# Optimization experiments

Hardware: AMD Instinct MI355X
Metric: run time of the kernel (lower is better)

## Reference

```python
import jax, jax.numpy as jnp
import numpy as np
from jax import lax

KSIZE = 3      # match kernel
STRIDE = 1
RATE = 2       # dilation / downscale rate
FUSE_K = 3     # diagonal-fuse kernel
SCALE = 10.0   # softmax scale
FUSE = True
ESC = 1e-4     # escape_NaN, added per-element before the reduce_sum (as in torch code)


def _same_pad(x, k, s):
    # x: [C, H, W] -> zero-padded so that strided k-window 'same' extraction works
    C, H, W = x.shape
    oh, ow = -(-H // s), -(-W // s)
    ph = max(0, (oh - 1) * s + k - H)
    pw = max(0, (ow - 1) * s + k - W)
    xp = jnp.pad(x, ((0, 0), (ph // 2, ph - ph // 2), (pw // 2, pw - pw // 2)))
    return xp, oh, ow


def extract_patches(x, k, s):
    # x: [C, H, W] -> [L, C, k, k], L row-major over output grid (matches torch Unfold)
    C = x.shape[0]
    xp, oh, ow = _same_pad(x, k, s)
    cols = [xp[:, dh:dh + s * (oh - 1) + 1:s, dw:dw + s * (ow - 1) + 1:s]
            for dh in range(k) for dw in range(k)]
    p = jnp.stack(cols, 0).reshape(k, k, C, oh, ow)
    return p.transpose(3, 4, 2, 0, 1).reshape(oh * ow, C, k, k)


def fuse_diag(x):
    # conv with eye(FUSE_K) kernel, 'same' padding: sum of diagonal shifts
    A, B = x.shape
    pt = (FUSE_K - 1) // 2
    pb = FUSE_K - 1 - pt
    xp = jnp.pad(x, ((pt, pb), (pt, pb)))
    out = xp[0:A, 0:B]
    for d in range(1, FUSE_K):
        out = out + xp[d:d + A, d:d + B]
    return out


def _forward(f, b, mask):
    B, C, H, W = f.shape
    kernel = 2 * RATE
    # mask -> mm gate over background patches (shared across batch: torch uses m[0])
    mask_s = mask[0][:, ::4 * RATE, ::4 * RATE]           # [1, H/r, W/r] nearest downsample
    m = extract_patches(mask_s, KSIZE, STRIDE)            # [L, 1, k, k]
    mm = (jnp.mean(m, axis=(1, 2, 3)) == 0.0).astype(f.dtype)[:, None, None]  # [L,1,1]

    def single(fi, bi):
        # raw patches from full-res background for reconstruction: [Lb, C, 2r, 2r]
        raw_w = extract_patches(bi, kernel, RATE * STRIDE)
        # nearest 1/rate downsample
        fs = fi[:, ::RATE, ::RATE]
        bs = bi[:, ::RATE, ::RATE]
        bh, bw = bs.shape[1], bs.shape[2]
        fh, fw = fs.shape[1], fs.shape[2]
        Lb, Lf = bh * bw, fh * fw
        # match patches from downsampled background, L2-normalized per patch
        w = extract_patches(bs, KSIZE, STRIDE)                      # [Lb, C, 3, 3]
        denom = jnp.sqrt(jnp.sum(w * w + ESC, axis=(1, 2, 3), keepdims=True))
        wn = (w / denom).reshape(Lb, -1)                            # [Lb, C*9]
        # correlation = conv of fs with wn filters = patch GEMM
        fp = extract_patches(fs, KSIZE, 1).reshape(Lf, -1)          # [Lf, C*9]
        scores = wn @ fp.T                                          # [Lb, Lf]
        if FUSE:
            s = fuse_diag(scores)
            s = s.reshape(bh, bw, fh, fw).transpose(1, 0, 3, 2).reshape(Lb, Lf)
            s = fuse_diag(s)
            s = s.reshape(bw, bh, fw, fh).transpose(1, 0, 3, 2).reshape(Lb, Lf)
            scores = s
        att = scores.reshape(Lb, fh, fw) * mm
        att = jax.nn.softmax(att * SCALE, axis=0) * mm              # softmax over patches
        # conv_transpose2d(att, raw_w, stride=rate, padding=1) / 4
        rhs = jnp.flip(raw_w, (2, 3)).transpose(1, 0, 2, 3)         # [C, Lb, 2r, 2r] OIHW
        pad = kernel - 1 - 1                                        # k - 1 - torch_padding
        out = lax.conv_general_dilated(
            att[None], rhs, window_strides=(1, 1),
            padding=[(pad, pad), (pad, pad)], lhs_dilation=(RATE, RATE),
            dimension_numbers=('NCHW', 'OIHW', 'NCHW'))[0] / 4.0    # [C, H, W]
        return out

    return jax.vmap(single)(f, b)


def setup_inputs() -> dict:
    key = jax.random.key(0)
    k1, k2 = jax.random.split(key)
    B, C, H, W = 4, 128, 96, 96
    f = jax.random.normal(k1, (B, C, H, W), jnp.float32)
    b = jax.random.normal(k2, (B, C, H, W), jnp.float32)
    mask = jnp.zeros((1, 1, 4 * H, 4 * W), jnp.float32)
    mask = mask.at[:, :, 96:288, 96:288].set(1.0)
    return {"f": f, "b": b, "mask": mask}


def reference(f, b, mask):
    return _forward(f, b, mask)
```

## Files before the change

kernel.cpp:

```cpp
#include <hip/hip_runtime.h>

typedef _Float16 half8 __attribute__((ext_vector_type(8)));
typedef float floatx4 __attribute__((ext_vector_type(4)));

#define LBF 2304
#define K1  1152
#define LDK2 2304

__device__ __forceinline__ void gll16(const _Float16* g, _Float16* l) {
    __builtin_amdgcn_global_load_lds((const __attribute__((address_space(1))) void*)g,
                                     (__attribute__((address_space(3))) void*)l, 16, 0, 0);
}

__device__ __forceinline__ int dec_kc(int s) { return (s >= 0) ? s + 1 : -s - 1; }

__global__ void prep_fp(const float* __restrict__ f, _Float16* __restrict__ fp) {
    int k = blockIdx.x * 128 + threadIdx.x;
    int p = blockIdx.y;
    int b = blockIdx.z;
    int c = k / 9, r = k % 9, u = r / 3, v = r % 3;
    int pi = p / 48, pj = p % 48;
    int y = pi - 1 + u, x = pj - 1 + v;
    float val = 0.f;
    if ((unsigned)y < 48u && (unsigned)x < 48u)
        val = f[(((long)b * 128 + c) * 96 + 2 * y) * 96 + 2 * x];
    fp[((long)b * LBF + p) * K1 + k] = (_Float16)val;
}

__global__ void prep_wn(const float* __restrict__ bsrc, _Float16* __restrict__ wn) {
    int p = blockIdx.x, b = blockIdx.y;
    int tid = threadIdx.x;
    int pi = p / 48, pj = p % 48;
    float w[9];
    float ss = 0.f;
#pragma unroll
    for (int t = 0; t < 9; t++) {
        int k = tid + t * 128;
        int c = k / 9, r = k % 9, u = r / 3, v = r % 3;
        int y = pi - 1 + u, x = pj - 1 + v;
        float val = 0.f;
        if ((unsigned)y < 48u && (unsigned)x < 48u)
            val = bsrc[(((long)b * 128 + c) * 96 + 2 * y) * 96 + 2 * x];
        w[t] = val;
        ss += val * val;
    }
    for (int m = 32; m; m >>= 1) ss += __shfl_xor(ss, m);
    __shared__ float sh[2];
    if ((tid & 63) == 0) sh[tid >> 6] = ss;
    __syncthreads();
    float denom = sqrtf(sh[0] + sh[1] + 0.1152f);
    float inv = 1.f / denom;
#pragma unroll
    for (int t = 0; t < 9; t++) {
        int k = tid + t * 128;
        wn[((long)b * LBF + p) * K1 + k] = (_Float16)(w[t] * inv);
    }
}

__global__ void scan_mm(const float* __restrict__ mask, int* __restrict__ pos) {
    int tid = threadIdx.x;
    int mmb[9], loc[9]; int s = 0;
#pragma unroll
    for (int t = 0; t < 9; t++) {
        int p = tid * 9 + t;
        int pi = p / 48, pj = p % 48;
        float sm = 0.f;
#pragma unroll
        for (int u = 0; u < 3; u++)
#pragma unroll
            for (int v = 0; v < 3; v++) {
                int y = pi - 1 + u, x = pj - 1 + v;
                if ((unsigned)y < 48u && (unsigned)x < 48u)
                    sm += mask[(8 * y) * 384 + 8 * x];
            }
        int m = (sm == 0.f) ? 1 : 0;
        mmb[t] = m; loc[t] = s; s += m;
    }
    __shared__ int sh[256];
    sh[tid] = s; __syncthreads();
    for (int off = 1; off < 256; off <<= 1) {
        int v = (tid >= off) ? sh[tid - off] : 0;
        __syncthreads();
        sh[tid] += v;
        __syncthreads();
    }
    int excl = sh[tid] - s;
#pragma unroll
    for (int t = 0; t < 9; t++) {
        int e = excl + loc[t];
        pos[tid * 9 + t] = mmb[t] ? e : (-e - 1);
    }
}

__global__ void prep_wtc(const float* __restrict__ bsrc, const int* __restrict__ pos,
                         _Float16* __restrict__ wtc) {
    int p = blockIdx.x * 256 + threadIdx.x;
    int n = blockIdx.y;
    int b = blockIdx.z;
    int sp = pos[p];
    if (sp < 0) return;
    int c = n >> 4, u = (n >> 2) & 3, v = n & 3;
    int pi = p / 48, pj = p % 48;
    int y = 2 * pi - 1 + u, x = 2 * pj - 1 + v;
    float val = 0.f;
    if ((unsigned)y < 96u && (unsigned)x < 96u)
        val = bsrc[(((long)b * 128 + c) * 96 + y) * 96 + x];
    wtc[((long)b * 2048 + n) * LDK2 + sp] = (_Float16)val;
}

__global__ void pad_zero(_Float16* __restrict__ buf, const int* __restrict__ pos) {
    int row = blockIdx.x;
    int kc = dec_kc(pos[2303]);
    int kp = (kc + 63) & ~63;
    int col = kc + threadIdx.x;
    if (col < kp) buf[(long)row * LDK2 + col] = (_Float16)0.f;
}

__device__ __forceinline__ void gemm_compute(const _Float16* lA, const _Float16* lB,
                                             floatx4 (&acc)[4][4],
                                             int wr, int wc, int lm, int pcp) {
    half8 af[4], bf[4];
#pragma unroll
    for (int t = 0; t < 4; t++) {
        af[t] = *(const half8*)&lA[(wr * 64 + t * 16 + lm) * 64 + pcp];
        bf[t] = *(const half8*)&lB[(wc * 64 + t * 16 + lm) * 64 + pcp];
    }
#pragma unroll
    for (int i = 0; i < 4; i++)
#pragma unroll
        for (int j = 0; j < 4; j++)
            acc[i][j] = __builtin_amdgcn_mfma_f32_16x16x32_f16(af[i], bf[j], acc[i][j], 0, 0, 0);
#pragma unroll
    for (int t = 0; t < 4; t++) {
        af[t] = *(const half8*)&lA[(wr * 64 + t * 16 + lm) * 64 + (pcp ^ 32)];
        bf[t] = *(const half8*)&lB[(wc * 64 + t * 16 + lm) * 64 + (pcp ^ 32)];
    }
#pragma unroll
    for (int i = 0; i < 4; i++)
#pragma unroll
        for (int j = 0; j < 4; j++)
            acc[i][j] = __builtin_amdgcn_mfma_f32_16x16x32_f16(af[i], bf[j], acc[i][j], 0, 0, 0);
}

__global__ __launch_bounds__(256)
void gemm_nt64(const _Float16* __restrict__ A, const _Float16* __restrict__ B,
               float* __restrict__ C, int M, int N, int ldk,
               const int* __restrict__ Kpos, int Kstat, long sA, long sB, long sC) {
    A += blockIdx.z * sA; B += blockIdx.z * sB; C += blockIdx.z * sC;
    int K;
    if (Kpos) { int kc = dec_kc(Kpos[0]); K = (kc + 63) & ~63; }
    else K = Kstat;
    const int tid = threadIdx.x;
    const int lane = tid & 63, wave = tid >> 6;
    const int wr = wave >> 1, wc = wave & 1;
    const int m0 = blockIdx.y * 128, n0 = blockIdx.x * 128;

    __shared__ _Float16 sm[4][128 * 64];

    floatx4 acc[4][4] = {};

    const int lm = lane & 15, q = lane >> 4;
    const int pcp = (q ^ (lm & 7)) * 8;

    const int srow8 = lane >> 3;
    const int gc = ((lane & 7) ^ srow8) * 8;
    const _Float16* gA[4]; const _Float16* gB[4];
    int dOff[4];
#pragma unroll
    for (int c = 0; c < 4; c++) {
        int r = (wave * 4 + c) * 8 + srow8;
        gA[c] = A + (long)(m0 + r) * ldk + gc;
        gB[c] = B + (long)(n0 + r) * ldk + gc;
        dOff[c] = (wave * 4 + c) * 512;
    }

    if (K > 0) {
#pragma unroll
        for (int c = 0; c < 4; c++) gll16(gA[c], &sm[0][dOff[c]]);
#pragma unroll
        for (int c = 0; c < 4; c++) gll16(gB[c], &sm[1][dOff[c]]);
        __syncthreads();
        int k0 = 0, buf = 0;
        while (true) {
            int kn = k0 + 64;
            if (kn < K) {
                const int nb = (buf ^ 1) * 2;
#pragma unroll
                for (int c = 0; c < 4; c++) gll16(gA[c] + kn, &sm[nb][dOff[c]]);
#pragma unroll
                for (int c = 0; c < 4; c++) gll16(gB[c] + kn, &sm[nb + 1][dOff[c]]);
            }
            gemm_compute(sm[buf * 2], sm[buf * 2 + 1], acc, wr, wc, lm, pcp);
            __syncthreads();
            k0 = kn; buf ^= 1;
            if (k0 >= K) break;
        }
    }

    const int col = n0 + wc * 64 + lm;
    const int rowq = q * 4;
#pragma unroll
    for (int i = 0; i < 4; i++) {
        int row = m0 + wr * 64 + i * 16 + rowq;
#pragma unroll
        for (int j = 0; j < 4; j++)
#pragma unroll
            for (int r = 0; r < 4; r++)
                C[(long)(row + r) * N + col + j * 16] = acc[i][j][r];
    }
}

__global__ __launch_bounds__(256)
void fuseA(const float* __restrict__ ST, float* __restrict__ FT1) {
    int y = blockIdx.x, bb = blockIdx.y;
    const float* S = ST + (long)bb * LBF * LBF;
    float* F = FT1 + (long)bb * LBF * LBF;
    const float* r0 = S + (long)(y > 0 ? y - 1 : 0) * LBF;
    const float* r1 = S + (long)y * LBF;
    const float* r2 = S + (long)(y < LBF - 1 ? y + 1 : y) * LBF;
    float m0 = (y > 0) ? 1.f : 0.f;
    float m2 = (y < LBF - 1) ? 1.f : 0.f;
    float* o = F + (long)y * LBF;
#pragma unroll
    for (int u = 0; u < 9; u++) {
        int x = threadIdx.x + u * 256;
        float lo = (x > 0) ? m0 * r0[x - 1] : 0.f;
        float hi = (x < LBF - 1) ? m2 * r2[x + 1] : 0.f;
        o[x] = lo + r1[x] + hi;
    }
}

__global__ __launch_bounds__(256)
void fuseB_softmax(const float* __restrict__ FT1, const int* __restrict__ pos,
                   _Float16* __restrict__ attTc_g) {
    int j = blockIdx.x, bb = blockIdx.y;
    int tid = threadIdx.x;
    const float* F = FT1 + (long)bb * LBF * LBF;
    _Float16* orow = attTc_g + ((long)bb * LBF + j) * LDK2;
    int Pj = (j % 48) * 48 + j / 48;
    long roff[3]; bool jok[3];
#pragma unroll
    for (int t = 0; t < 3; t++) {
        int j2 = Pj + t - 1;
        jok[t] = (unsigned)j2 < (unsigned)LBF;
        int jc = jok[t] ? j2 : 0;
        roff[t] = (long)((jc % 48) * 48 + jc / 48) * LBF;
    }
    float v[9]; int ps[9];
    float mx = -1e30f;
#pragma unroll
    for (int u = 0; u < 9; u++) {
        int x = tid + u * 256;
        int sp = pos[x];
        ps[u] = sp;
        float xv = 0.f;
        if (sp >= 0) {
            int a = x / 48, b = x - a * 48;
            int Px = b * 48 + a;
            float acc = 0.f;
#pragma unroll
            for (int t = 0; t < 3; t++) {
                int d2 = t - 1;
                int uu = Px + d2;
                if (jok[t] && (unsigned)uu < (unsigned)LBF) {
                    int ad = a + d2;
                    int c = ((unsigned)ad < 48u) ? (x + 48 * d2)
                          : (ad == 48 ? (b + 1) : (2255 + b));
                    acc += F[roff[t] + c];
                }
            }
            xv = acc * 10.f;
        }
        v[u] = xv;
        mx = fmaxf(mx, xv);
    }
    for (int m = 32; m; m >>= 1) mx = fmaxf(mx, __shfl_xor(mx, m));
    __shared__ float sh[4], sh2[4];
    if ((tid & 63) == 0) sh[tid >> 6] = mx;
    __syncthreads();
    mx = fmaxf(fmaxf(sh[0], sh[1]), fmaxf(sh[2], sh[3]));
    float sum = 0.f;
#pragma unroll
    for (int u = 0; u < 9; u++) { v[u] = __expf(v[u] - mx); sum += v[u]; }
    for (int m = 32; m; m >>= 1) sum += __shfl_xor(sum, m);
    if ((tid & 63) == 0) sh2[tid >> 6] = sum;
    __syncthreads();
    sum = sh2[0] + sh2[1] + sh2[2] + sh2[3];
    float inv = 1.f / sum;
#pragma unroll
    for (int u = 0; u < 9; u++) {
        if (ps[u] >= 0) orow[ps[u]] = (_Float16)(v[u] * inv);
    }
    int kc = dec_kc(pos[2303]);
    int kp = (kc + 63) & ~63;
    if (tid < kp - kc) orow[kc + tid] = (_Float16)0.f;
}

__global__ void scatter_out(const float* __restrict__ MT_, float* __restrict__ out) {
    int yx = blockIdx.x * 256 + threadIdx.x;
    int c = blockIdx.y, b = blockIdx.z;
    int y = yx / 96, x = yx % 96;
    const float* Mb = MT_ + (long)b * 2048 * LBF;
    float s = 0.f;
    for (int uu = (y + 1) & 1; uu < 4; uu += 2) {
        int fi = (y + 1 - uu) >> 1;
        if ((unsigned)fi >= 48u) continue;
        for (int vv = (x + 1) & 1; vv < 4; vv += 2) {
            int fj = (x + 1 - vv) >> 1;
            if ((unsigned)fj >= 48u) continue;
            s += Mb[(long)(c * 16 + uu * 4 + vv) * LBF + fi * 48 + fj];
        }
    }
    out[(((long)b * 128 + c) * 96 + y) * 96 + x] = 0.25f * s;
}

extern "C" void kernel_launch(void* const* d_in, const int* in_sizes, int n_in,
                              void* d_out, int out_size, void* d_ws, size_t ws_size,
                              hipStream_t stream) {
    const float* f    = (const float*)d_in[0];
    const float* bsrc = (const float*)d_in[1];
    const float* mask = (const float*)d_in[2];
    float* out = (float*)d_out;

    char* ws = (char*)d_ws;
    const size_t offR1  = 84934656;
    const size_t offWn  = offR1 + 21233664;
    const size_t offWtc = offR1 + 42467328;
    const size_t offFT1 = offWtc + 37748736;
    const size_t offPos = offFT1 + 2ul * 21233664;
    const size_t NEED   = offPos + 9216;
    if (ws_size < NEED) return;

    float*    ST    = (float*)(ws + 0);
    float*    MT    = (float*)(ws + 0);
    _Float16* fp    = (_Float16*)(ws + offR1);
    _Float16* wn    = (_Float16*)(ws + offWn);
    _Float16* attTc = (_Float16*)(ws + offR1);
    _Float16* Wtc   = (_Float16*)(ws + offWtc);
    float*    FT1   = (float*)(ws + offFT1);
    int*      pos   = (int*)(ws + offPos);

    scan_mm<<<dim3(1), 256, 0, stream>>>(mask, pos);
    prep_fp<<<dim3(9, 2304, 4), 128, 0, stream>>>(f, fp);
    prep_wn<<<dim3(2304, 4), 128, 0, stream>>>(bsrc, wn);
    prep_wtc<<<dim3(9, 2048, 4), 256, 0, stream>>>(bsrc, pos, Wtc);
    pad_zero<<<dim3(4 * 2048), 64, 0, stream>>>(Wtc, pos);

    gemm_nt64<<<dim3(18, 18, 4), 256, 0, stream>>>(fp, wn, ST, 2304, 2304, K1,
        nullptr, K1, (long)2304 * K1, (long)2304 * K1, (long)2304 * 2304);

    for (int g = 0; g < 2; g++) {
        fuseA<<<dim3(LBF, 2), 256, 0, stream>>>(ST + (long)g * 2 * LBF * LBF, FT1);
        fuseB_softmax<<<dim3(LBF, 2), 256, 0, stream>>>(FT1, pos,
            attTc + (long)g * 2 * LBF * LDK2);
    }

    gemm_nt64<<<dim3(18, 16, 4), 256, 0, stream>>>(Wtc, attTc, MT, 2048, 2304, LDK2,
        pos + 2303, 0, (long)2048 * LDK2, (long)2304 * LDK2, (long)2048 * 2304);

    scatter_out<<<dim3(36, 128, 4), 256, 0, stream>>>(MT, out);
}
```

Baseline: 497.6 us.

## Stage downsampled inputs, fold pad zeroing into prep_wtc, swap GEMM block order

Adds a staging kernel that writes the stride-2 downsampled f and b into a compact buffer, so prep_fp and prep_wn read dense data instead of strided full-resolution reads. The separate pad_zero launch is removed and its zeroing of the padded K tail is done by the masked-out threads of prep_wtc. The second GEMM gets a flag that swaps which grid axis maps to M and N, changing the order blocks are scheduled in for cache reuse. The staging buffer reuses the FT1 workspace region, and the tail-zeroing now relies on the masked positions being numerous enough to cover the pad width.

Result: faster. 474.2 us (-4.7%).

```diff
diff --git a/kernel.cpp b/kernel.cpp
--- a/kernel.cpp
+++ b/kernel.cpp
@@ -14,7 +14,20 @@
 
 __device__ __forceinline__ int dec_kc(int s) { return (s >= 0) ? s + 1 : -s - 1; }
 
-__global__ void prep_fp(const float* __restrict__ f, _Float16* __restrict__ fp) {
+__global__ void stage_ds(const float* __restrict__ f, const float* __restrict__ bsrc,
+                         float* __restrict__ ds) {
+    long flat = (long)blockIdx.x * 256 + threadIdx.x;
+    int p = flat % 2304;
+    long rest = flat / 2304;
+    int c = rest % 128;
+    int b = (rest / 128) % 4;
+    int t = rest / (128 * 4);
+    int pi = p / 48, pj = p % 48;
+    const float* src = t ? bsrc : f;
+    ds[flat] = src[(((long)b * 128 + c) * 96 + 2 * pi) * 96 + 2 * pj];
+}
+
+__global__ void prep_fp(const float* __restrict__ ds, _Float16* __restrict__ fp) {
     int k = blockIdx.x * 128 + threadIdx.x;
     int p = blockIdx.y;
     int b = blockIdx.z;
@@ -23,14 +36,15 @@
     int y = pi - 1 + u, x = pj - 1 + v;
     float val = 0.f;
     if ((unsigned)y < 48u && (unsigned)x < 48u)
-        val = f[(((long)b * 128 + c) * 96 + 2 * y) * 96 + 2 * x];
+        val = ds[((long)(b * 128 + c)) * 2304 + y * 48 + x];
     fp[((long)b * LBF + p) * K1 + k] = (_Float16)val;
 }
 
-__global__ void prep_wn(const float* __restrict__ bsrc, _Float16* __restrict__ wn) {
+__global__ void prep_wn(const float* __restrict__ ds, _Float16* __restrict__ wn) {
     int p = blockIdx.x, b = blockIdx.y;
     int tid = threadIdx.x;
     int pi = p / 48, pj = p % 48;
+    const float* dsb = ds + (long)(4 + b) * 128 * 2304;
     float w[9];
     float ss = 0.f;
 #pragma unroll
@@ -40,7 +54,7 @@
         int y = pi - 1 + u, x = pj - 1 + v;
         float val = 0.f;
         if ((unsigned)y < 48u && (unsigned)x < 48u)
-            val = bsrc[(((long)b * 128 + c) * 96 + 2 * y) * 96 + 2 * x];
+            val = dsb[(long)c * 2304 + y * 48 + x];
         w[t] = val;
         ss += val * val;
     }
@@ -98,7 +112,14 @@
     int n = blockIdx.y;
     int b = blockIdx.z;
     int sp = pos[p];
-    if (sp < 0) return;
+    if (sp < 0) {
+        int kc = dec_kc(pos[2303]);
+        int kp = (kc + 63) & ~63;
+        int mo = p + sp + 1;
+        if (mo < kp - kc)
+            wtc[((long)b * 2048 + n) * LDK2 + kc + mo] = (_Float16)0.f;
+        return;
+    }
     int c = n >> 4, u = (n >> 2) & 3, v = n & 3;
     int pi = p / 48, pj = p % 48;
     int y = 2 * pi - 1 + u, x = 2 * pj - 1 + v;
@@ -108,14 +129,6 @@
     wtc[((long)b * 2048 + n) * LDK2 + sp] = (_Float16)val;
 }
 
-__global__ void pad_zero(_Float16* __restrict__ buf, const int* __restrict__ pos) {
-    int row = blockIdx.x;
-    int kc = dec_kc(pos[2303]);
-    int kp = (kc + 63) & ~63;
-    int col = kc + threadIdx.x;
-    if (col < kp) buf[(long)row * LDK2 + col] = (_Float16)0.f;
-}
-
 __device__ __forceinline__ void gemm_compute(const _Float16* lA, const _Float16* lB,
                                              floatx4 (&acc)[4][4],
                                              int wr, int wc, int lm, int pcp) {
@@ -144,7 +157,7 @@
 
 __global__ __launch_bounds__(256)
 void gemm_nt64(const _Float16* __restrict__ A, const _Float16* __restrict__ B,
-               float* __restrict__ C, int M, int N, int ldk,
+               float* __restrict__ C, int M, int N, int ldk, int swapxy,
                const int* __restrict__ Kpos, int Kstat, long sA, long sB, long sC) {
     A += blockIdx.z * sA; B += blockIdx.z * sB; C += blockIdx.z * sC;
     int K;
@@ -153,7 +166,9 @@
     const int tid = threadIdx.x;
     const int lane = tid & 63, wave = tid >> 6;
     const int wr = wave >> 1, wc = wave & 1;
-    const int m0 = blockIdx.y * 128, n0 = blockIdx.x * 128;
+    const int bm = swapxy ? blockIdx.x : blockIdx.y;
+    const int bn = swapxy ? blockIdx.y : blockIdx.x;
+    const int m0 = bm * 128, n0 = bn * 128;
 
     __shared__ _Float16 sm[4][128 * 64];
 
@@ -337,16 +352,17 @@
     _Float16* wn    = (_Float16*)(ws + offWn);
     _Float16* attTc = (_Float16*)(ws + offR1);
     _Float16* Wtc   = (_Float16*)(ws + offWtc);
+    float*    ds    = (float*)(ws + offFT1);
     float*    FT1   = (float*)(ws + offFT1);
     int*      pos   = (int*)(ws + offPos);
 
+    stage_ds<<<dim3(9216), 256, 0, stream>>>(f, bsrc, ds);
     scan_mm<<<dim3(1), 256, 0, stream>>>(mask, pos);
-    prep_fp<<<dim3(9, 2304, 4), 128, 0, stream>>>(f, fp);
-    prep_wn<<<dim3(2304, 4), 128, 0, stream>>>(bsrc, wn);
+    prep_fp<<<dim3(9, 2304, 4), 128, 0, stream>>>(ds, fp);
+    prep_wn<<<dim3(2304, 4), 128, 0, stream>>>(ds, wn);
     prep_wtc<<<dim3(9, 2048, 4), 256, 0, stream>>>(bsrc, pos, Wtc);
-    pad_zero<<<dim3(4 * 2048), 64, 0, stream>>>(Wtc, pos);
-
-    gemm_nt64<<<dim3(18, 18, 4), 256, 0, stream>>>(fp, wn, ST, 2304, 2304, K1,
+
+    gemm_nt64<<<dim3(18, 18, 4), 256, 0, stream>>>(fp, wn, ST, 2304, 2304, K1, 0,
         nullptr, K1, (long)2304 * K1, (long)2304 * K1, (long)2304 * 2304);
 
     for (int g = 0; g < 2; g++) {
@@ -355,7 +371,7 @@
             attTc + (long)g * 2 * LBF * LDK2);
     }
 
-    gemm_nt64<<<dim3(18, 16, 4), 256, 0, stream>>>(Wtc, attTc, MT, 2048, 2304, LDK2,
+    gemm_nt64<<<dim3(16, 18, 4), 256, 0, stream>>>(Wtc, attTc, MT, 2048, 2304, LDK2, 1,
         pos + 2303, 0, (long)2048 * LDK2, (long)2304 * LDK2, (long)2048 * 2304);
 
     scatter_out<<<dim3(36, 128, 4), 256, 0, stream>>>(MT, out);
```
